# Kernel optimization log

Measured on AMD Instinct MI355X. Metric: run time of the kernel, lower is better.

Reference implementation:

```python
import jax, jax.numpy as jnp
import numpy as np

D_MODEL = 1024
H = 16
D_K = D_MODEL // H
D_FF = 4096
EPS = 1e-6
NEG = -1e9


def layernorm(x, alpha, bias):
    # custom LN: unbiased std (ddof=1), scalar alpha/bias, divide by (std+eps)
    mean = jnp.mean(x, axis=-1, keepdims=True)
    n = x.shape[-1]
    var = jnp.sum((x - mean) ** 2, axis=-1, keepdims=True) / (n - 1)
    std = jnp.sqrt(var)
    return alpha * (x - mean) / (std + EPS) + bias


def setup_inputs() -> dict:
    key = jax.random.key(0)
    ks = jax.random.split(key, 16)
    B, S = 2, 2048
    s = 1.0 / np.sqrt(D_MODEL)
    inp = {
        "x": jax.random.normal(ks[0], (B, S, D_MODEL), jnp.float32),
        "src_mask": jnp.ones((B, 1, S), jnp.int32),
        "wq": jax.random.normal(ks[1], (D_MODEL, D_MODEL), jnp.float32) * s,
        "bq": jnp.zeros((D_MODEL,), jnp.float32),
        "wk": jax.random.normal(ks[2], (D_MODEL, D_MODEL), jnp.float32) * s,
        "bk": jnp.zeros((D_MODEL,), jnp.float32),
        "wv": jax.random.normal(ks[3], (D_MODEL, D_MODEL), jnp.float32) * s,
        "bv": jnp.zeros((D_MODEL,), jnp.float32),
        "wo": jax.random.normal(ks[4], (D_MODEL, D_MODEL), jnp.float32) * s,
        "bo": jnp.zeros((D_MODEL,), jnp.float32),
        "w1": jax.random.normal(ks[5], (D_MODEL, D_FF), jnp.float32) * s,
        "b1": jnp.zeros((D_FF,), jnp.float32),
        "w2": jax.random.normal(ks[6], (D_FF, D_MODEL), jnp.float32) * (1.0 / np.sqrt(D_FF)),
        "b2": jnp.zeros((D_MODEL,), jnp.float32),
        "ln1_a": jnp.ones((1,), jnp.float32),
        "ln1_b": jnp.zeros((1,), jnp.float32),
        "ln2_a": jnp.ones((1,), jnp.float32),
        "ln2_b": jnp.zeros((1,), jnp.float32),
    }
    return inp


def reference(x, src_mask, wq, bq, wk, bk, wv, bv, wo, bo,
              w1, b1, w2, b2, ln1_a, ln1_b, ln2_a, ln2_b):
    B, S, _ = x.shape
    # --- residual 1: pre-norm self attention ---
    xn = layernorm(x, ln1_a, ln1_b)
    q = (xn @ wq + bq).reshape(B, S, H, D_K)
    k = (xn @ wk + bk).reshape(B, S, H, D_K)
    v = (xn @ wv + bv).reshape(B, S, H, D_K)
    # scores [B, H, S, S]
    scores = jnp.einsum("bqhd,bkhd->bhqk", q, k) / jnp.sqrt(jnp.float32(D_K))
    m = src_mask[:, None, :, :]  # [B,1,1,S]
    scores = jnp.where(m == 0, NEG, scores)
    attn = jax.nn.softmax(scores, axis=-1)
    ctx = jnp.einsum("bhqk,bkhd->bqhd", attn, v).reshape(B, S, D_MODEL)
    attn_out = ctx @ wo + bo
    x = x + attn_out
    # --- residual 2: pre-norm FFN ---
    xn = layernorm(x, ln2_a, ln2_b)
    ff = jax.nn.relu(xn @ w1 + b1) @ w2 + b2
    return x + ff
```

## Files before the change

### kernel.cpp

```cpp
#include <hip/hip_runtime.h>
#include <hip/hip_bf16.h>

typedef __attribute__((ext_vector_type(8))) short short8;
typedef __attribute__((ext_vector_type(4))) float f32x4;
using u16 = unsigned short;
typedef unsigned int u32;

__device__ __forceinline__ u16 f2bf(float f) {
    u32 u = __builtin_bit_cast(u32, f);
    u32 r = u + 0x7FFFu + ((u >> 16) & 1u);
    return (u16)(r >> 16);
}

__device__ __forceinline__ void async_load16(const void* g, void* l) {
    __builtin_amdgcn_global_load_lds(
        (const __attribute__((address_space(1))) void*)g,
        (__attribute__((address_space(3))) void*)l, 16, 0, 0);
}

__global__ __launch_bounds__(256) void convt_kernel(const float* __restrict__ w,
                                                    u16* __restrict__ wt, int K, int N) {
    __shared__ float tile[32][33];
    int bn = blockIdx.x * 32, bk = blockIdx.y * 32;
    int tx = threadIdx.x & 31, ty = threadIdx.x >> 5;
#pragma unroll
    for (int i = 0; i < 4; i++)
        tile[ty + i * 8][tx] = w[(size_t)(bk + ty + i * 8) * N + bn + tx];
    __syncthreads();
#pragma unroll
    for (int i = 0; i < 4; i++)
        wt[(size_t)(bn + ty + i * 8) * K + bk + tx] = f2bf(tile[tx][ty + i * 8]);
}

__global__ __launch_bounds__(256) void vtrans_kernel(const u16* __restrict__ qkv,
                                                     u16* __restrict__ vT) {
    __shared__ u16 tile[32][33];
    int bs = blockIdx.x * 32;
    int bc = blockIdx.y * 32;
    int b  = blockIdx.z;
    int tx = threadIdx.x & 31, ty = threadIdx.x >> 5;
#pragma unroll
    for (int i = 0; i < 4; i++)
        tile[ty + i * 8][tx] = qkv[(size_t)(b * 2048 + bs + ty + i * 8) * 3072 + 2048 + bc + tx];
    __syncthreads();
#pragma unroll
    for (int i = 0; i < 4; i++)
        vT[(size_t)(b * 1024 + bc + ty + i * 8) * 2048 + bs + tx] = tile[tx][ty + i * 8];
}

__global__ __launch_bounds__(256) void ln_kernel(const float* __restrict__ x,
                                                 const float* __restrict__ ga,
                                                 const float* __restrict__ gb,
                                                 u16* __restrict__ out) {
    int row = blockIdx.x;
    const float4* xr = (const float4*)(x + (size_t)row * 1024);
    float4 v = xr[threadIdx.x];
    float s  = v.x + v.y + v.z + v.w;
    float s2 = v.x * v.x + v.y * v.y + v.z * v.z + v.w * v.w;
#pragma unroll
    for (int off = 32; off; off >>= 1) {
        s  += __shfl_down(s, off);
        s2 += __shfl_down(s2, off);
    }
    __shared__ float rs[4], rs2[4];
    int wid = threadIdx.x >> 6, lane = threadIdx.x & 63;
    if (lane == 0) { rs[wid] = s; rs2[wid] = s2; }
    __syncthreads();
    float S  = rs[0] + rs[1] + rs[2] + rs[3];
    float S2 = rs2[0] + rs2[1] + rs2[2] + rs2[3];
    float mean = S * (1.0f / 1024.0f);
    float var  = fmaxf((S2 - 1024.0f * mean * mean) * (1.0f / 1023.0f), 0.0f);
    float scale = ga[0] / (sqrtf(var) + 1e-6f);
    float shift = gb[0] - mean * scale;
    u16 h0 = f2bf(v.x * scale + shift);
    u16 h1 = f2bf(v.y * scale + shift);
    u16 h2 = f2bf(v.z * scale + shift);
    u16 h3 = f2bf(v.w * scale + shift);
    uint2 pv;
    pv.x = (u32)h0 | ((u32)h1 << 16);
    pv.y = (u32)h2 | ((u32)h3 << 16);
    *(uint2*)(out + (size_t)row * 1024 + threadIdx.x * 4) = pv;
}

__global__ __launch_bounds__(256) void bias3_kernel(const float* __restrict__ a,
                                                    const float* __restrict__ b,
                                                    const float* __restrict__ c,
                                                    float* __restrict__ d) {
    int i = blockIdx.x * 256 + threadIdx.x;
    float v = (i < 1024) ? a[i] : ((i < 2048) ? b[i - 1024] : c[i - 2048]);
    d[i] = v;
}

__global__ __launch_bounds__(256) void addbias_kernel(float* __restrict__ dst,
                                                      const float* __restrict__ p,
                                                      const float* __restrict__ bias,
                                                      const float* __restrict__ resid) {
    int i4 = blockIdx.x * 256 + threadIdx.x;
    float4 d  = ((const float4*)dst)[i4];
    float4 pp = ((const float4*)p)[i4];
    float4 rr = ((const float4*)resid)[i4];
    float4 bb = *(const float4*)(bias + ((i4 * 4) & 1023));
    d.x += pp.x + bb.x + rr.x;
    d.y += pp.y + bb.y + rr.y;
    d.z += pp.z + bb.z + rr.z;
    d.w += pp.w + bb.w + rr.w;
    ((float4*)dst)[i4] = d;
}

template <int MODE, int RELU, int RESID>
__global__ __launch_bounds__(256) void gemm_bt(const u16* __restrict__ A,
                                               const u16* __restrict__ Bt,
                                               const float* __restrict__ bias,
                                               void* __restrict__ C0,
                                               void* __restrict__ C1,
                                               const float* __restrict__ resid,
                                               int M, int N, int K, int kLen) {
    __shared__ u16 As[8192];
    __shared__ u16 Bs[8192];
    int tid = threadIdx.x, lane = tid & 63, wid = tid >> 6;
    int l15 = lane & 15, l4 = lane >> 4;
    int rowA0 = blockIdx.x * 128;
    int rowB0 = blockIdx.y * 128;
    int kOff = blockIdx.z * kLen;
    void* Cout = blockIdx.z ? C1 : C0;
    int waveM = wid >> 1, waveN = wid & 1;

    int fl = tid * 8;
    int r0 = fl >> 5, c0 = fl & 31;
    const u16* gA0 = A + (size_t)(rowA0 + r0) * K + c0 + kOff;
    const u16* gA1 = A + (size_t)(rowA0 + 64 + r0) * K + c0 + kOff;
    const u16* gB0 = Bt + (size_t)(rowB0 + r0) * K + c0 + kOff;
    const u16* gB1 = Bt + (size_t)(rowB0 + 64 + r0) * K + c0 + kOff;

    f32x4 acc[4][4] = {};
    const int nIter = kLen >> 5;

    async_load16(gA0, As + wid * 512);
    async_load16(gA1, As + 2048 + wid * 512);
    async_load16(gB0, Bs + wid * 512);
    async_load16(gB1, Bs + 2048 + wid * 512);

    int cur = 0, kb = 32;
    for (int it = 0; it < nIter; ++it) {
        asm volatile("s_waitcnt vmcnt(0)" ::: "memory");
        __builtin_amdgcn_s_barrier();
        if (it + 1 < nIter) {
            u16* a = As + (cur ^ 1) * 4096;
            u16* bb = Bs + (cur ^ 1) * 4096;
            async_load16(gA0 + kb, a + wid * 512);
            async_load16(gA1 + kb, a + 2048 + wid * 512);
            async_load16(gB0 + kb, bb + wid * 512);
            async_load16(gB1 + kb, bb + 2048 + wid * 512);
        }
        __builtin_amdgcn_sched_barrier(0);

        const u16* a = As + cur * 4096;
        const u16* bb = Bs + cur * 4096;
        short8 af[4], bf[4];
#pragma unroll
        for (int m = 0; m < 4; m++)
            af[m] = *(const short8*)&a[(waveM * 64 + m * 16 + l15) * 32 + l4 * 8];
#pragma unroll
        for (int n = 0; n < 4; n++)
            bf[n] = *(const short8*)&bb[(waveN * 64 + n * 16 + l15) * 32 + l4 * 8];
#pragma unroll
        for (int m = 0; m < 4; m++)
#pragma unroll
            for (int n = 0; n < 4; n++)
                acc[m][n] = __builtin_amdgcn_mfma_f32_16x16x32_bf16(af[m], bf[n], acc[m][n], 0, 0, 0);

        __builtin_amdgcn_s_barrier();
        cur ^= 1;
        kb += 32;
    }

#pragma unroll
    for (int m = 0; m < 4; m++) {
        int row = rowA0 + waveM * 64 + m * 16 + l4 * 4;
#pragma unroll
        for (int n = 0; n < 4; n++) {
            int col = rowB0 + waveN * 64 + n * 16 + l15;
            float bc = (MODE == 2) ? 0.0f : bias[col];
#pragma unroll
            for (int j = 0; j < 4; j++) {
                float v = acc[m][n][j] + bc;
                if (RELU) v = fmaxf(v, 0.0f);
                if (RESID) v += resid[(size_t)(row + j) * N + col];
                if (MODE == 1)
                    ((u16*)Cout)[(size_t)(row + j) * N + col] = f2bf(v);
                else
                    ((float*)Cout)[(size_t)(row + j) * N + col] = v;
            }
        }
    }
}

__global__ __launch_bounds__(256) void attn_kernel(const u16* __restrict__ qkv,
                                                   const u16* __restrict__ vT,
                                                   const int* __restrict__ mask,
                                                   u16* __restrict__ ctx) {
    const int S = 2048;
    const float SCALE = 0.125f;
    int qt = blockIdx.x;
    int bh = blockIdx.y;
    int b = bh >> 4, h = bh & 15;
    int tid = threadIdx.x;
    int wid = tid >> 6, lane = tid & 63;
    int l15 = lane & 15, l4 = lane >> 4;

    __shared__ u16 Ks[64][72];
    __shared__ u16 Vs[64][72];
    __shared__ u16 Plds[4][16][72];
    __shared__ int mflag;

    if (tid == 0) mflag = 1;
    __syncthreads();
    {
        const int* mrow = mask + b * S;
        int ok = 1;
#pragma unroll
        for (int i = 0; i < 8; i++) ok &= (mrow[tid * 8 + i] != 0);
        if (!ok) mflag = 0;
    }

    int qrow0 = qt * 64 + wid * 16;
    const u16* qb = qkv + (size_t)(b * S + qrow0) * 3072 + h * 64;
    short8 qf0 = *(const short8*)(qb + (size_t)l15 * 3072 + l4 * 8);
    short8 qf1 = *(const short8*)(qb + (size_t)l15 * 3072 + 32 + l4 * 8);

    f32x4 o[4] = {};
    float m_i[4], lp[4];
#pragma unroll
    for (int j = 0; j < 4; j++) { m_i[j] = -1e30f; lp[j] = 0.0f; }
    __syncthreads();
    const int allones = mflag;
    const int* mrow = mask + b * S;

    int srow = tid >> 3, c8 = (tid & 7) * 8;
    short8 kreg[2], vreg[2];
#pragma unroll
    for (int p = 0; p < 2; p++) {
        int r = p * 32 + srow;
        kreg[p] = *(const short8*)(qkv + (size_t)(b * S + r) * 3072 + 1024 + h * 64 + c8);
        vreg[p] = *(const short8*)(vT + (size_t)(bh * 64 + r) * 2048 + c8);
    }

    for (int kt = 0; kt < 32; ++kt) {
        __builtin_amdgcn_s_barrier();
#pragma unroll
        for (int p = 0; p < 2; p++) {
            int r = p * 32 + srow;
            *(short8*)&Ks[r][c8] = kreg[p];
            *(short8*)&Vs[r][c8] = vreg[p];
        }
        if (kt + 1 < 32) {
#pragma unroll
            for (int p = 0; p < 2; p++) {
                int r = p * 32 + srow;
                kreg[p] = *(const short8*)(qkv + (size_t)(b * S + (kt + 1) * 64 + r) * 3072 + 1024 + h * 64 + c8);
                vreg[p] = *(const short8*)(vT + (size_t)(bh * 64 + r) * 2048 + (kt + 1) * 64 + c8);
            }
        }
        asm volatile("s_waitcnt lgkmcnt(0)" ::: "memory");
        __builtin_amdgcn_s_barrier();

        float sc[4][4];
#pragma unroll
        for (int kc = 0; kc < 4; kc++) {
            short8 kf0 = *(const short8*)&Ks[kc * 16 + l15][l4 * 8];
            short8 kf1 = *(const short8*)&Ks[kc * 16 + l15][32 + l4 * 8];
            f32x4 a = {};
            a = __builtin_amdgcn_mfma_f32_16x16x32_bf16(qf0, kf0, a, 0, 0, 0);
            a = __builtin_amdgcn_mfma_f32_16x16x32_bf16(qf1, kf1, a, 0, 0, 0);
            if (allones) {
#pragma unroll
                for (int j = 0; j < 4; j++) sc[kc][j] = a[j] * SCALE;
            } else {
                int mk = mrow[kt * 64 + kc * 16 + l15];
#pragma unroll
                for (int j = 0; j < 4; j++) sc[kc][j] = mk ? a[j] * SCALE : -1e9f;
            }
        }

        float lm[4];
#pragma unroll
        for (int j = 0; j < 4; j++)
            lm[j] = fmaxf(fmaxf(sc[0][j], sc[1][j]), fmaxf(sc[2][j], sc[3][j]));
        bool ok2 = (lm[0] <= m_i[0] + 8.0f) && (lm[1] <= m_i[1] + 8.0f) &&
                   (lm[2] <= m_i[2] + 8.0f) && (lm[3] <= m_i[3] + 8.0f);
        if (!__all(ok2)) {
#pragma unroll
            for (int j = 0; j < 4; j++) {
                float t = lm[j];
#pragma unroll
                for (int mm = 8; mm >= 1; mm >>= 1) t = fmaxf(t, __shfl_xor(t, mm, 16));
                float newm = fmaxf(m_i[j], t);
                float r = __expf(m_i[j] - newm);
                lp[j] *= r;
#pragma unroll
                for (int dc = 0; dc < 4; dc++) o[dc][j] *= r;
                m_i[j] = newm;
            }
        }
#pragma unroll
        for (int j = 0; j < 4; j++) {
#pragma unroll
            for (int kc = 0; kc < 4; kc++) {
                float p = __expf(sc[kc][j] - m_i[j]);
                lp[j] += p;
                Plds[wid][l4 * 4 + j][kc * 16 + l15] = f2bf(p);
            }
        }

        short8 pa0 = *(const short8*)&Plds[wid][l15][l4 * 8];
        short8 pa1 = *(const short8*)&Plds[wid][l15][32 + l4 * 8];
#pragma unroll
        for (int dc = 0; dc < 4; dc++) {
            short8 vf0 = *(const short8*)&Vs[dc * 16 + l15][l4 * 8];
            short8 vf1 = *(const short8*)&Vs[dc * 16 + l15][32 + l4 * 8];
            o[dc] = __builtin_amdgcn_mfma_f32_16x16x32_bf16(pa0, vf0, o[dc], 0, 0, 0);
            o[dc] = __builtin_amdgcn_mfma_f32_16x16x32_bf16(pa1, vf1, o[dc], 0, 0, 0);
        }
    }

#pragma unroll
    for (int j = 0; j < 4; j++) {
        float s = lp[j];
#pragma unroll
        for (int mm = 8; mm >= 1; mm >>= 1) s += __shfl_xor(s, mm, 16);
        float inv = 1.0f / s;
        int row = qrow0 + l4 * 4 + j;
        size_t base = (size_t)(b * S + row) * 1024 + h * 64;
#pragma unroll
        for (int dc = 0; dc < 4; dc++)
            ctx[base + dc * 16 + l15] = f2bf(o[dc][j] * inv);
    }
}

extern "C" void kernel_launch(void* const* d_in, const int* in_sizes, int n_in,
                              void* d_out, int out_size, void* d_ws, size_t ws_size,
                              hipStream_t stream) {
    const float* x    = (const float*)d_in[0];
    const int*   mask = (const int*)d_in[1];
    const float* wq   = (const float*)d_in[2];
    const float* bq   = (const float*)d_in[3];
    const float* wk   = (const float*)d_in[4];
    const float* bk   = (const float*)d_in[5];
    const float* wv   = (const float*)d_in[6];
    const float* bv   = (const float*)d_in[7];
    const float* wo   = (const float*)d_in[8];
    const float* bo   = (const float*)d_in[9];
    const float* w1   = (const float*)d_in[10];
    const float* b1   = (const float*)d_in[11];
    const float* w2   = (const float*)d_in[12];
    const float* b2   = (const float*)d_in[13];
    const float* ln1a = (const float*)d_in[14];
    const float* ln1b = (const float*)d_in[15];
    const float* ln2a = (const float*)d_in[16];
    const float* ln2b = (const float*)d_in[17];
    float* out = (float*)d_out;

    char* ws = (char*)d_ws;
    u16*   wqkvt = (u16*)(ws + 0);
    u16*   wot   = (u16*)(ws + 6291456);
    u16*   w1t   = (u16*)(ws + 8388608);
    u16*   w2t   = (u16*)(ws + 16777216);
    float* bqkv  = (float*)(ws + 25165824);
    char*  regA  = ws + 26214400;
    u16*   xn1   = (u16*)(regA + 0);
    u16*   vT    = (u16*)(regA + 0);
    u16*   qkv   = (u16*)(regA + 8388608);
    u16*   ctx   = (u16*)(regA + 33554432);
    float* p0wo  = (float*)(regA + 0);
    float* x1    = (float*)(ws + 68157440);
    u16*   xn2   = (u16*)(regA + 0);
    u16*   ff1   = (u16*)(regA + 8388608);
    float* p0f2  = (float*)(ws + 0);

    dim3 blk(256);

    convt_kernel<<<dim3(32, 32), blk, 0, stream>>>(wq, wqkvt, 1024, 1024);
    convt_kernel<<<dim3(32, 32), blk, 0, stream>>>(wk, wqkvt + 1024 * 1024, 1024, 1024);
    convt_kernel<<<dim3(32, 32), blk, 0, stream>>>(wv, wqkvt + 2048 * 1024, 1024, 1024);
    convt_kernel<<<dim3(32, 32), blk, 0, stream>>>(wo, wot, 1024, 1024);
    convt_kernel<<<dim3(128, 32), blk, 0, stream>>>(w1, w1t, 1024, 4096);
    convt_kernel<<<dim3(32, 128), blk, 0, stream>>>(w2, w2t, 4096, 1024);
    bias3_kernel<<<dim3(12), blk, 0, stream>>>(bq, bk, bv, bqkv);

    ln_kernel<<<dim3(4096), blk, 0, stream>>>(x, ln1a, ln1b, xn1);
    gemm_bt<1, 0, 0><<<dim3(32, 24, 1), blk, 0, stream>>>(xn1, wqkvt, bqkv, qkv, qkv, nullptr,
                                                          4096, 3072, 1024, 1024);
    vtrans_kernel<<<dim3(64, 32, 2), blk, 0, stream>>>(qkv, vT);
    attn_kernel<<<dim3(32, 32), blk, 0, stream>>>(qkv, vT, mask, ctx);
    gemm_bt<2, 0, 0><<<dim3(32, 8, 2), blk, 0, stream>>>(ctx, wot, nullptr, p0wo, x1, nullptr,
                                                         4096, 1024, 1024, 512);
    addbias_kernel<<<dim3(4096), blk, 0, stream>>>(x1, p0wo, bo, x);

    ln_kernel<<<dim3(4096), blk, 0, stream>>>(x1, ln2a, ln2b, xn2);
    gemm_bt<1, 1, 0><<<dim3(32, 32, 1), blk, 0, stream>>>(xn2, w1t, b1, ff1, ff1, nullptr,
                                                          4096, 4096, 1024, 1024);
    gemm_bt<2, 0, 0><<<dim3(32, 8, 2), blk, 0, stream>>>(ff1, w2t, nullptr, p0f2, out, nullptr,
                                                         4096, 1024, 4096, 2048);
    addbias_kernel<<<dim3(4096), blk, 0, stream>>>(out, p0f2, b2, x1);
}
```

Baseline: 293.5 us.

## Transpose attention score MFMA, use exp2 softmax with packed bf16 P, merge weight converts

The QK^T MFMA operands are swapped so each lane holds scores for a single query row. This lets the running max and sum become scalars per lane, reduced with two cross-lane shuffles. The 1/sqrt(d) scale is folded into a log2(e) constant so the exponentials use the hardware exp2, and probabilities are packed to bf16 with v_cvt_pk_bf16_f32 into a transposed u32 LDS tile. The rescale threshold is loosened, and the four 1024x1024 weight conversion launches are merged into one kernel. In exchange, the output rescale and normalisation now need extra lane shuffles.

```diff
diff --git a/kernel.cpp b/kernel.cpp
--- a/kernel.cpp
+++ b/kernel.cpp
@@ -3,6 +3,7 @@
 
 typedef __attribute__((ext_vector_type(8))) short short8;
 typedef __attribute__((ext_vector_type(4))) float f32x4;
+typedef __attribute__((ext_vector_type(4))) unsigned int u32x4;
 using u16 = unsigned short;
 typedef unsigned int u32;
 
@@ -10,6 +11,16 @@
     u32 u = __builtin_bit_cast(u32, f);
     u32 r = u + 0x7FFFu + ((u >> 16) & 1u);
     return (u16)(r >> 16);
+}
+
+__device__ __forceinline__ float exp2fast(float x) {
+    return __builtin_amdgcn_exp2f(x);
+}
+
+__device__ __forceinline__ u32 cvtpk(float lo, float hi) {
+    u32 r;
+    asm("v_cvt_pk_bf16_f32 %0, %1, %2" : "=v"(r) : "v"(lo), "v"(hi));
+    return r;
 }
 
 __device__ __forceinline__ void async_load16(const void* g, void* l) {
@@ -30,6 +41,29 @@
 #pragma unroll
     for (int i = 0; i < 4; i++)
         wt[(size_t)(bn + ty + i * 8) * K + bk + tx] = f2bf(tile[tx][ty + i * 8]);
+}
+
+__global__ __launch_bounds__(256) void convt4_kernel(const float* __restrict__ wa,
+                                                     const float* __restrict__ wb,
+                                                     const float* __restrict__ wc,
+                                                     const float* __restrict__ wd,
+                                                     u16* __restrict__ da,
+                                                     u16* __restrict__ db,
+                                                     u16* __restrict__ dc,
+                                                     u16* __restrict__ dd) {
+    __shared__ float tile[32][33];
+    int z = blockIdx.z;
+    const float* w = (z == 0) ? wa : (z == 1) ? wb : (z == 2) ? wc : wd;
+    u16* wt = (z == 0) ? da : (z == 1) ? db : (z == 2) ? dc : dd;
+    int bn = blockIdx.x * 32, bk = blockIdx.y * 32;
+    int tx = threadIdx.x & 31, ty = threadIdx.x >> 5;
+#pragma unroll
+    for (int i = 0; i < 4; i++)
+        tile[ty + i * 8][tx] = w[(size_t)(bk + ty + i * 8) * 1024 + bn + tx];
+    __syncthreads();
+#pragma unroll
+    for (int i = 0; i < 4; i++)
+        wt[(size_t)(bn + ty + i * 8) * 1024 + bk + tx] = f2bf(tile[tx][ty + i * 8]);
 }
 
 __global__ __launch_bounds__(256) void vtrans_kernel(const u16* __restrict__ qkv,
@@ -200,7 +234,7 @@
                                                    const int* __restrict__ mask,
                                                    u16* __restrict__ ctx) {
     const int S = 2048;
-    const float SCALE = 0.125f;
+    const float C = 0.180336880f;
     int qt = blockIdx.x;
     int bh = blockIdx.y;
     int b = bh >> 4, h = bh & 15;
@@ -210,7 +244,7 @@
 
     __shared__ u16 Ks[64][72];
     __shared__ u16 Vs[64][72];
-    __shared__ u16 Plds[4][16][72];
+    __shared__ u32 PT[4][16][38];
     __shared__ int mflag;
 
     if (tid == 0) mflag = 1;
@@ -229,9 +263,7 @@
     short8 qf1 = *(const short8*)(qb + (size_t)l15 * 3072 + 32 + l4 * 8);
 
     f32x4 o[4] = {};
-    float m_i[4], lp[4];
-#pragma unroll
-    for (int j = 0; j < 4; j++) { m_i[j] = -1e30f; lp[j] = 0.0f; }
+    float m_i = -1e30f, lp = 0.0f;
     __syncthreads();
     const int allones = mflag;
     const int* mrow = mask + b * S;
@@ -270,50 +302,66 @@
             short8 kf0 = *(const short8*)&Ks[kc * 16 + l15][l4 * 8];
             short8 kf1 = *(const short8*)&Ks[kc * 16 + l15][32 + l4 * 8];
             f32x4 a = {};
-            a = __builtin_amdgcn_mfma_f32_16x16x32_bf16(qf0, kf0, a, 0, 0, 0);
-            a = __builtin_amdgcn_mfma_f32_16x16x32_bf16(qf1, kf1, a, 0, 0, 0);
+            a = __builtin_amdgcn_mfma_f32_16x16x32_bf16(kf0, qf0, a, 0, 0, 0);
+            a = __builtin_amdgcn_mfma_f32_16x16x32_bf16(kf1, qf1, a, 0, 0, 0);
             if (allones) {
 #pragma unroll
-                for (int j = 0; j < 4; j++) sc[kc][j] = a[j] * SCALE;
+                for (int j = 0; j < 4; j++) sc[kc][j] = a[j];
             } else {
-                int mk = mrow[kt * 64 + kc * 16 + l15];
-#pragma unroll
-                for (int j = 0; j < 4; j++) sc[kc][j] = mk ? a[j] * SCALE : -1e9f;
+#pragma unroll
+                for (int j = 0; j < 4; j++) {
+                    int mk = mrow[kt * 64 + kc * 16 + l4 * 4 + j];
+                    sc[kc][j] = mk ? a[j] : -1e9f;
+                }
             }
         }
 
-        float lm[4];
-#pragma unroll
-        for (int j = 0; j < 4; j++)
-            lm[j] = fmaxf(fmaxf(sc[0][j], sc[1][j]), fmaxf(sc[2][j], sc[3][j]));
-        bool ok2 = (lm[0] <= m_i[0] + 8.0f) && (lm[1] <= m_i[1] + 8.0f) &&
-                   (lm[2] <= m_i[2] + 8.0f) && (lm[3] <= m_i[3] + 8.0f);
-        if (!__all(ok2)) {
-#pragma unroll
-            for (int j = 0; j < 4; j++) {
-                float t = lm[j];
-#pragma unroll
-                for (int mm = 8; mm >= 1; mm >>= 1) t = fmaxf(t, __shfl_xor(t, mm, 16));
-                float newm = fmaxf(m_i[j], t);
-                float r = __expf(m_i[j] - newm);
-                lp[j] *= r;
-#pragma unroll
-                for (int dc = 0; dc < 4; dc++) o[dc][j] *= r;
-                m_i[j] = newm;
+        float lm = sc[0][0];
+#pragma unroll
+        for (int kc = 0; kc < 4; kc++)
+#pragma unroll
+            for (int j = 0; j < 4; j++) lm = fmaxf(lm, sc[kc][j]);
+        if (!__all(lm <= m_i + 64.0f)) {
+            float t = lm;
+            t = fmaxf(t, __shfl_xor(t, 16));
+            t = fmaxf(t, __shfl_xor(t, 32));
+            float newm = fmaxf(m_i, t);
+            float r = exp2fast((m_i - newm) * C);
+            lp *= r;
+            float rr0 = __shfl(r, l4 * 4 + 0);
+            float rr1 = __shfl(r, l4 * 4 + 1);
+            float rr2 = __shfl(r, l4 * 4 + 2);
+            float rr3 = __shfl(r, l4 * 4 + 3);
+#pragma unroll
+            for (int dc = 0; dc < 4; dc++) {
+                o[dc][0] *= rr0; o[dc][1] *= rr1; o[dc][2] *= rr2; o[dc][3] *= rr3;
             }
-        }
-#pragma unroll
-        for (int j = 0; j < 4; j++) {
-#pragma unroll
-            for (int kc = 0; kc < 4; kc++) {
-                float p = __expf(sc[kc][j] - m_i[j]);
-                lp[j] += p;
-                Plds[wid][l4 * 4 + j][kc * 16 + l15] = f2bf(p);
-            }
-        }
-
-        short8 pa0 = *(const short8*)&Plds[wid][l15][l4 * 8];
-        short8 pa1 = *(const short8*)&Plds[wid][l15][32 + l4 * 8];
+            m_i = newm;
+        }
+
+        float nb = -m_i * C;
+#pragma unroll
+        for (int kc = 0; kc < 4; kc++) {
+            float p0 = exp2fast(fmaf(sc[kc][0], C, nb));
+            float p1 = exp2fast(fmaf(sc[kc][1], C, nb));
+            float p2 = exp2fast(fmaf(sc[kc][2], C, nb));
+            float p3 = exp2fast(fmaf(sc[kc][3], C, nb));
+            lp += (p0 + p1) + (p2 + p3);
+            uint2 w;
+            w.x = cvtpk(p0, p1);
+            w.y = cvtpk(p2, p3);
+            *(uint2*)&PT[wid][l15][kc * 8 + l4 * 2] = w;
+        }
+
+        uint2 r01 = *(const uint2*)&PT[wid][l15][l4 * 4];
+        uint2 r23 = *(const uint2*)&PT[wid][l15][l4 * 4 + 2];
+        uint2 r45 = *(const uint2*)&PT[wid][l15][16 + l4 * 4];
+        uint2 r67 = *(const uint2*)&PT[wid][l15][16 + l4 * 4 + 2];
+        u32x4 w0 = {r01.x, r01.y, r23.x, r23.y};
+        u32x4 w1 = {r45.x, r45.y, r67.x, r67.y};
+        short8 pa0 = __builtin_bit_cast(short8, w0);
+        short8 pa1 = __builtin_bit_cast(short8, w1);
+
 #pragma unroll
         for (int dc = 0; dc < 4; dc++) {
             short8 vf0 = *(const short8*)&Vs[dc * 16 + l15][l4 * 8];
@@ -323,17 +371,22 @@
         }
     }
 
+    float lt = lp;
+    lt += __shfl_xor(lt, 16);
+    lt += __shfl_xor(lt, 32);
+    float inv = 1.0f / lt;
+    float iv0 = __shfl(inv, l4 * 4 + 0);
+    float iv1 = __shfl(inv, l4 * 4 + 1);
+    float iv2 = __shfl(inv, l4 * 4 + 2);
+    float iv3 = __shfl(inv, l4 * 4 + 3);
 #pragma unroll
     for (int j = 0; j < 4; j++) {
-        float s = lp[j];
-#pragma unroll
-        for (int mm = 8; mm >= 1; mm >>= 1) s += __shfl_xor(s, mm, 16);
-        float inv = 1.0f / s;
+        float ivj = (j == 0) ? iv0 : (j == 1) ? iv1 : (j == 2) ? iv2 : iv3;
         int row = qrow0 + l4 * 4 + j;
         size_t base = (size_t)(b * S + row) * 1024 + h * 64;
 #pragma unroll
         for (int dc = 0; dc < 4; dc++)
-            ctx[base + dc * 16 + l15] = f2bf(o[dc][j] * inv);
+            ctx[base + dc * 16 + l15] = f2bf(o[dc][j] * ivj);
     }
 }
 
@@ -379,10 +432,8 @@
 
     dim3 blk(256);
 
-    convt_kernel<<<dim3(32, 32), blk, 0, stream>>>(wq, wqkvt, 1024, 1024);
-    convt_kernel<<<dim3(32, 32), blk, 0, stream>>>(wk, wqkvt + 1024 * 1024, 1024, 1024);
-    convt_kernel<<<dim3(32, 32), blk, 0, stream>>>(wv, wqkvt + 2048 * 1024, 1024, 1024);
-    convt_kernel<<<dim3(32, 32), blk, 0, stream>>>(wo, wot, 1024, 1024);
+    convt4_kernel<<<dim3(32, 32, 4), blk, 0, stream>>>(
+        wq, wk, wv, wo, wqkvt, wqkvt + 1024 * 1024, wqkvt + 2048 * 1024, wot);
     convt_kernel<<<dim3(128, 32), blk, 0, stream>>>(w1, w1t, 1024, 4096);
     convt_kernel<<<dim3(32, 128), blk, 0, stream>>>(w2, w2t, 4096, 1024);
     bias3_kernel<<<dim3(12), blk, 0, stream>>>(bq, bk, bv, bqkv);
```

New measurement: 277.0 us. 5.6% less time.
